# Optimization experiments

Hardware: AMD Instinct MI355X
Metric: run time of the kernel (lower is better)

Reference implementation:

```python
import jax, jax.numpy as jnp
import numpy as np

K = 512          # patch size
H = 16           # heads
C = 768          # dim
ROPE_BASE = 100.0
COUNTS = [8000, 8300, 7800, 8668]


def _build_pad_unpad(counts, k):
    # faithful numpy replica of EfficientAttentionV2.get_padding_and_inverse
    counts = np.asarray(counts, dtype=np.int64)
    cpad = np.where(counts > k, ((counts + k - 1) // k) * k, counts)
    off = np.concatenate([[0], np.cumsum(counts)])
    offp = np.concatenate([[0], np.cumsum(cpad)])
    pad = np.arange(offp[-1])
    unpad = np.arange(off[-1])
    for i in range(len(counts)):
        unpad[off[i]:off[i + 1]] += offp[i] - off[i]
        if counts[i] != cpad[i]:
            s = offp[i + 1] - k + counts[i] % k
            pad[s:offp[i + 1]] = pad[s - k:offp[i + 1] - k]
        pad[offp[i]:offp[i + 1]] -= offp[i] - off[i]
    return pad, unpad


def setup_inputs() -> dict:
    key = jax.random.key(0)
    ks = jax.random.split(key, 6)
    N = int(np.sum(COUNTS))
    pad, unpad = _build_pad_unpad(COUNTS, K)
    rng = np.random.default_rng(0)
    perm = rng.permutation(N)                 # serialized_order stand-in
    inv_perm = np.argsort(perm)               # serialized_inverse
    order = perm[pad].astype(np.int32)        # [N_pad]
    inverse = unpad[inv_perm].astype(np.int32)  # [N]
    grid = rng.integers(0, 1024, size=(N, 3))
    pos = grid[order].astype(np.int32)        # [N_pad, 3], gathered grid coords
    s = 0.02
    return {
        "x": jax.random.normal(ks[0], (N, C), jnp.float32),
        "w_qkv": jax.random.normal(ks[1], (C, 3 * C), jnp.float32) * s,
        "b_qkv": jnp.zeros((3 * C,), jnp.float32),
        "w_proj": jax.random.normal(ks[2], (C, C), jnp.float32) * s,
        "b_proj": jnp.zeros((C,), jnp.float32),
        "order": jnp.asarray(order),
        "inverse": jnp.asarray(inverse),
        "pos": jnp.asarray(pos),
    }


def _rope1d(tok, pos1d):
    # tok: [P, K, H, d], pos1d: [P, K]
    d = tok.shape[-1]
    inv_freq = 1.0 / (ROPE_BASE ** (jnp.arange(0, d, 2, dtype=jnp.float32) / d))
    fr = pos1d[..., None].astype(jnp.float32) * inv_freq      # [P, K, d/2]
    fr = jnp.concatenate([fr, fr], axis=-1)[:, :, None, :]    # [P, K, 1, d]
    x1, x2 = jnp.split(tok, 2, axis=-1)
    rot = jnp.concatenate([-x2, x1], axis=-1)
    return tok * jnp.cos(fr) + rot * jnp.sin(fr)


def _rope3d(tok, pos):
    # tok: [P, K, H, D]; pos: [P, K, 3]; split head dim into 3 axis chunks
    parts = jnp.split(tok, 3, axis=-1)
    return jnp.concatenate(
        [_rope1d(parts[i], pos[..., i]) for i in range(3)], axis=-1)


def reference(x, w_qkv, b_qkv, w_proj, b_proj, order, inverse, pos):
    D = C // H
    scale = D ** -0.5
    qkv = x @ w_qkv + b_qkv                     # [N, 3C]
    qkv = qkv[order]                            # [N_pad, 3C] patch gather
    qkv = qkv.reshape(-1, K, 3, H, D)           # [P, K, 3, H, D]
    q, k, v = qkv[:, :, 0], qkv[:, :, 1], qkv[:, :, 2]  # [P, K, H, D]
    ppos = pos.reshape(-1, K, 3)
    q = _rope3d(q, ppos)
    k = _rope3d(k, ppos)
    attn = jnp.einsum("pkhd,pmhd->phkm", q, k) * scale
    attn = jax.nn.softmax(attn, axis=-1)
    feat = jnp.einsum("phkm,pmhd->pkhd", attn, v).reshape(-1, C)  # [N_pad, C]
    feat = feat[inverse]                        # [N, C] scatter-back
    return feat @ w_proj + b_proj
```

## Files before the change

kernel.cpp:

```cpp
#include <hip/hip_runtime.h>
#include <stdint.h>

typedef short short8 __attribute__((ext_vector_type(8)));
typedef short short4v __attribute__((ext_vector_type(4)));
typedef float f32x4 __attribute__((ext_vector_type(4)));
typedef float f32x16 __attribute__((ext_vector_type(16)));

#define AS1C(p) ((const __attribute__((address_space(1))) unsigned int*)(p))
#define AS3(p)  ((__attribute__((address_space(3))) unsigned int*)(p))

__device__ __forceinline__ short f2bf(float f) {
  union { float f; unsigned u; } v; v.f = f;
  unsigned r = v.u + 0x7FFFu + ((v.u >> 16) & 1u);
  return (short)(r >> 16);
}

__global__ void k_cast_bf16(const float* __restrict__ src, short* __restrict__ dst, int n8) {
  const int i = blockIdx.x * 256 + threadIdx.x;
  if (i >= n8) return;
  const float4* s = (const float4*)src + (size_t)i * 2;
  const float4 a = s[0], b = s[1];
  short8 o;
  o[0] = f2bf(a.x); o[1] = f2bf(a.y); o[2] = f2bf(a.z); o[3] = f2bf(a.w);
  o[4] = f2bf(b.x); o[5] = f2bf(b.y); o[6] = f2bf(b.z); o[7] = f2bf(b.w);
  ((short8*)dst)[i] = o;
}

__global__ void k_transpose_cast(const float* __restrict__ src, short* __restrict__ dst,
                                 int R, int C) {
  __shared__ float t[32][33];
  const int tx = threadIdx.x & 31, ty = threadIdx.x >> 5;
  const int c0 = blockIdx.x * 32, r0 = blockIdx.y * 32;
#pragma unroll
  for (int j = 0; j < 4; ++j)
    t[ty + j * 8][tx] = src[(size_t)(r0 + ty + j * 8) * C + c0 + tx];
  __syncthreads();
#pragma unroll
  for (int j = 0; j < 4; ++j)
    dst[(size_t)(c0 + ty + j * 8) * R + r0 + tx] = f2bf(t[tx][ty + j * 8]);
}

__global__ __launch_bounds__(256, 2)
void k_gemm1(const short* __restrict__ x16, const short* __restrict__ wt,
             const float* __restrict__ bqkv, const int* __restrict__ order,
             const int* __restrict__ pos,
             short* __restrict__ Qp, short* __restrict__ Kp, short* __restrict__ VpT) {
  __shared__ short sA[128 * 64];
  __shared__ short sB[128 * 64];
  __shared__ int sOrd[128];

  const int tid = threadIdx.x;
  const int lane = tid & 63;
  const int wv = tid >> 6;
  const int wm = wv >> 1, wn = wv & 1;
  const int tm = blockIdx.x * 128;
  const int tn = blockIdx.y * 128;

  if (tid < 128) sOrd[tid] = order[tm + tid];
  __syncthreads();

  const char* srcA[4];
  const char* srcB[4];
  {
    const int rr = tid >> 3, ck = tid & 7;
    const int sc = (ck ^ (rr & 7)) * 16;
#pragma unroll
    for (int is = 0; is < 4; ++is) {
      srcA[is] = (const char*)(x16 + (size_t)sOrd[is * 32 + rr] * 768) + sc;
      srcB[is] = (const char*)(wt + (size_t)(tn + is * 32 + rr) * 768) + sc;
    }
  }

  f32x4 acc[4][4] = {};
  const int ldsw = wv << 10;

  for (int kk = 0; kk < 12; ++kk) {
    const int kb = kk << 7;
#pragma unroll
    for (int is = 0; is < 4; ++is)
      __builtin_amdgcn_global_load_lds(AS1C(srcA[is] + kb), AS3((char*)sA + is * 4096 + ldsw), 16, 0, 0);
#pragma unroll
    for (int is = 0; is < 4; ++is)
      __builtin_amdgcn_global_load_lds(AS1C(srcB[is] + kb), AS3((char*)sB + is * 4096 + ldsw), 16, 0, 0);
    __syncthreads();

#pragma unroll
    for (int kbl = 0; kbl < 2; ++kbl) {
      const int ko = kbl * 64 + ((lane >> 4) << 4);
      short8 af[4], bf[4];
#pragma unroll
      for (int mi = 0; mi < 4; ++mi) {
        int row = wm * 64 + mi * 16 + (lane & 15);
        af[mi] = *(const short8*)((const char*)sA + row * 128 + (ko ^ ((row & 7) << 4)));
      }
#pragma unroll
      for (int ni = 0; ni < 4; ++ni) {
        int row = wn * 64 + ni * 16 + (lane & 15);
        bf[ni] = *(const short8*)((const char*)sB + row * 128 + (ko ^ ((row & 7) << 4)));
      }
#pragma unroll
      for (int mi = 0; mi < 4; ++mi)
#pragma unroll
        for (int ni = 0; ni < 4; ++ni)
          acc[mi][ni] = __builtin_amdgcn_mfma_f32_16x16x32_bf16(af[mi], bf[ni], acc[mi][ni], 0, 0, 0);
    }
    __syncthreads();
  }

  const int which = tn / 768;
  if (which == 2) {
#pragma unroll
    for (int ni = 0; ni < 4; ++ni) {
      const int col = tn + wn * 64 + ni * 16 + (lane & 15);
      const int hcol = col - 1536;
      const int h = hcol / 48;
      const int dd = hcol % 48;
      const float bq = bqkv[col];
#pragma unroll
      for (int mi = 0; mi < 4; ++mi) {
        const int m0 = tm + wm * 64 + mi * 16 + ((lane >> 4) << 2);
        const int p = m0 >> 9, q0 = m0 & 511;
        short4v vv;
#pragma unroll
        for (int r = 0; r < 4; ++r) vv[r] = f2bf(acc[mi][ni][r] + bq);
        *(short4v*)(VpT + ((size_t)(p * 16 + h) * 48 + dd) * 512 + q0) = vv;
      }
    }
  } else {
    const float invf = exp2f(-(float)(lane & 7) * 0.830482023721840f);
#pragma unroll
    for (int ni = 0; ni < 4; ++ni) {
      const int col = tn + wn * 64 + ni * 16 + (lane & 15);
      const int hcol = col - which * 768;
      const int h = hcol / 48;
      const int dd = hcol % 48;
      const int part = dd >> 4;
      const float bq = bqkv[col];
#pragma unroll
      for (int mi = 0; mi < 4; ++mi) {
        const int m0 = tm + wm * 64 + mi * 16 + ((lane >> 4) << 2);
#pragma unroll
        for (int r = 0; r < 4; ++r) {
          const int m = m0 + r;
          float val = acc[mi][ni][r] + bq;
          const int pv = pos[m * 3 + part];
          float s, c;
          __sincosf((float)pv * invf, &s, &c);
          const float partner = __shfl_xor(val, 8);
          val = val * c + ((lane & 8) ? partner : -partner) * s;
          const int p = m >> 9, q = m & 511;
          const size_t ro = (size_t)(p * 16 + h) * 512 + q;
          if (which == 0) Qp[ro * 48 + dd] = f2bf(val);
          else            Kp[(ro << 6) + dd] = f2bf(val);
        }
      }
    }
  }
}

__global__ __launch_bounds__(512, 2)
void k_attn(const short* __restrict__ Qp, const short* __restrict__ Kp,
            const short* __restrict__ VpT, short* __restrict__ featp) {
  __shared__ short sK[2][64 * 64];
  __shared__ short sV[2][64 * 64];

  const int tid = threadIdx.x;
  const int lane = tid & 63;
  const int wv = tid >> 6;
  const int l31 = lane & 31;
  const int hi = lane >> 5;
  const int ph = blockIdx.x;
  const int p = ph >> 4, h = ph & 15;

  ((float*)((char*)sV[0] + 6144))[tid] = 0.0f;
  ((float*)((char*)sV[1] + 6144))[tid] = 0.0f;

  short8 qf[2][3];
  {
    const short* Qb = Qp + ((size_t)ph * 512 + wv * 64) * 48;
#pragma unroll
    for (int qt = 0; qt < 2; ++qt)
#pragma unroll
      for (int dk = 0; dk < 3; ++dk)
        qf[qt][dk] = *(const short8*)(Qb + (qt * 32 + l31) * 48 + dk * 16 + hi * 8);
  }

  const char* Kb = (const char*)Kp + (size_t)ph * 65536;
  const char* Vb = (const char*)VpT + (size_t)ph * 49152;
  const int ldsw = wv << 10;
  const int o = tid * 16;
  const int swK = o ^ ((o >> 3) & 0x70);
  const int dV = tid >> 3;
  const int inrowV = (o & 127) ^ ((o >> 3) & 0x70);

  auto stage = [&](int b, int ms) {
    __builtin_amdgcn_global_load_lds(AS1C(Kb + ms * 8192 + swK), AS3((char*)sK[b] + ldsw), 16, 0, 0);
    if (tid < 384)
      __builtin_amdgcn_global_load_lds(AS1C(Vb + (size_t)dV * 1024 + ms * 128 + inrowV),
                                       AS3((char*)sV[b] + ldsw), 16, 0, 0);
  };

  stage(0, 0);
  asm volatile("s_waitcnt vmcnt(0)" ::: "memory");
  __syncthreads();

  f32x16 O[2][2] = {};
  float lr[2] = {0.f, 0.f};
  const float K2 = 0.14433756729740644f * 1.4426950408889634f;
  const float MB = 8.0f * K2;

  for (int ms = 0; ms < 8; ++ms) {
    const int bb = ms & 1;
    if (ms < 7) stage(bb ^ 1, ms + 1);

    const char* kb = (const char*)sK[bb];
    const char* vb = (const char*)sV[bb];

    f32x16 st[2][2];
    {
      short8 kf[2][3];
#pragma unroll
      for (int mt = 0; mt < 2; ++mt) {
        const int row = mt * 32 + l31;
        const int swr = (row & 7) << 4;
#pragma unroll
        for (int dk = 0; dk < 3; ++dk) {
          const int ob = (dk * 16 + hi * 8) * 2;
          kf[mt][dk] = *(const short8*)(kb + row * 128 + (ob ^ swr));
        }
      }
      __builtin_amdgcn_s_setprio(1);
#pragma unroll
      for (int mt = 0; mt < 2; ++mt)
#pragma unroll
        for (int qt = 0; qt < 2; ++qt) {
          f32x16 a = {};
#pragma unroll
          for (int dk = 0; dk < 3; ++dk)
            a = __builtin_amdgcn_mfma_f32_32x32x16_bf16(kf[mt][dk], qf[qt][dk], a, 0, 0, 0);
          st[mt][qt] = a;
        }
      __builtin_amdgcn_s_setprio(0);
    }

    unsigned pk[2][2][8];
#pragma unroll
    for (int qt = 0; qt < 2; ++qt) {
      float ps = 0.f;
#pragma unroll
      for (int mt = 0; mt < 2; ++mt) {
#pragma unroll
        for (int pr = 0; pr < 8; ++pr) {
          float p0 = exp2f(st[mt][qt][pr * 2]     * K2 - MB);
          float p1 = exp2f(st[mt][qt][pr * 2 + 1] * K2 - MB);
          ps += p0 + p1;
          pk[mt][qt][pr] = (unsigned)(unsigned short)f2bf(p0) |
                           ((unsigned)(unsigned short)f2bf(p1) << 16);
        }
      }
      lr[qt] += ps;
    }

    short8 vf[2][4];
#pragma unroll
    for (int dt = 0; dt < 2; ++dt) {
      const int d = dt * 32 + l31;
      const int swr = (d & 7) << 4;
#pragma unroll
      for (int ks = 0; ks < 4; ++ks) {
        const int ob = (ks * 16 + hi * 8) * 2;
        vf[dt][ks] = *(const short8*)(vb + d * 128 + (ob ^ swr));
      }
    }
#pragma unroll
    for (int qt = 0; qt < 2; ++qt) {
#pragma unroll
      for (int ks = 0; ks < 4; ++ks) {
        const int mt = ks >> 1;
        const int b0 = (ks & 1) * 4;
        const unsigned X0 = pk[mt][qt][b0 + 0];
        const unsigned X1 = pk[mt][qt][b0 + 1];
        const unsigned Y0 = pk[mt][qt][b0 + 2];
        const unsigned Y1 = pk[mt][qt][b0 + 3];
        const unsigned tX0 = __shfl_xor(X0, 32);
        const unsigned tX1 = __shfl_xor(X1, 32);
        const unsigned tY0 = __shfl_xor(Y0, 32);
        const unsigned tY1 = __shfl_xor(Y1, 32);
        union { unsigned u[4]; short8 v; } aw;
        aw.u[0] = hi ? tY0 : X0;
        aw.u[1] = hi ? tY1 : X1;
        aw.u[2] = hi ? Y0 : tX0;
        aw.u[3] = hi ? Y1 : tX1;
        __builtin_amdgcn_s_setprio(1);
#pragma unroll
        for (int dt = 0; dt < 2; ++dt)
          O[qt][dt] = __builtin_amdgcn_mfma_f32_32x32x16_bf16(aw.v, vf[dt][ks], O[qt][dt], 0, 0, 0);
        __builtin_amdgcn_s_setprio(0);
      }
    }

    if (ms < 7) {
      asm volatile("s_waitcnt vmcnt(0)" ::: "memory");
      __syncthreads();
    }
  }

#pragma unroll
  for (int qt = 0; qt < 2; ++qt) {
    float l = lr[qt] + __shfl_xor(lr[qt], 32);
    const float il = 1.0f / l;
#pragma unroll
    for (int r = 0; r < 16; ++r) {
      const int crow = (r & 3) + ((r >> 2) << 3) + (hi << 2);
      const float ilr = __shfl(il, crow);
      const int qg = wv * 64 + qt * 32 + crow;
      const size_t base = ((size_t)(p * 512 + qg)) * 768 + h * 48;
      featp[base + l31] = f2bf(O[qt][0][r] * ilr);
      if (l31 < 16) featp[base + 32 + l31] = f2bf(O[qt][1][r] * ilr);
    }
  }
}

__global__ __launch_bounds__(256, 2)
void k_gemm2(const short* __restrict__ featp, const short* __restrict__ wt,
             const float* __restrict__ bproj, const int* __restrict__ inverse,
             float* __restrict__ out) {
  __shared__ short sA[128 * 64];
  __shared__ short sB[128 * 64];
  __shared__ int sInv[128];

  const int tid = threadIdx.x;
  const int lane = tid & 63;
  const int wv = tid >> 6;
  const int wm = wv >> 1, wn = wv & 1;
  const int tm = blockIdx.x * 128;
  const int tn = blockIdx.y * 128;

  if (tid < 128) sInv[tid] = inverse[tm + tid];
  __syncthreads();

  const char* srcA[4];
  const char* srcB[4];
  {
    const int rr = tid >> 3, ck = tid & 7;
    const int sc = (ck ^ (rr & 7)) * 16;
#pragma unroll
    for (int is = 0; is < 4; ++is) {
      srcA[is] = (const char*)(featp + (size_t)sInv[is * 32 + rr] * 768) + sc;
      srcB[is] = (const char*)(wt + (size_t)(tn + is * 32 + rr) * 768) + sc;
    }
  }

  f32x4 acc[4][4] = {};
  const int ldsw = wv << 10;

  for (int kk = 0; kk < 12; ++kk) {
    const int kb = kk << 7;
#pragma unroll
    for (int is = 0; is < 4; ++is)
      __builtin_amdgcn_global_load_lds(AS1C(srcA[is] + kb), AS3((char*)sA + is * 4096 + ldsw), 16, 0, 0);
#pragma unroll
    for (int is = 0; is < 4; ++is)
      __builtin_amdgcn_global_load_lds(AS1C(srcB[is] + kb), AS3((char*)sB + is * 4096 + ldsw), 16, 0, 0);
    __syncthreads();

#pragma unroll
    for (int kbl = 0; kbl < 2; ++kbl) {
      const int ko = kbl * 64 + ((lane >> 4) << 4);
      short8 af[4], bf[4];
#pragma unroll
      for (int mi = 0; mi < 4; ++mi) {
        int row = wm * 64 + mi * 16 + (lane & 15);
        af[mi] = *(const short8*)((const char*)sA + row * 128 + (ko ^ ((row & 7) << 4)));
      }
#pragma unroll
      for (int ni = 0; ni < 4; ++ni) {
        int row = wn * 64 + ni * 16 + (lane & 15);
        bf[ni] = *(const short8*)((const char*)sB + row * 128 + (ko ^ ((row & 7) << 4)));
      }
#pragma unroll
      for (int mi = 0; mi < 4; ++mi)
#pragma unroll
        for (int ni = 0; ni < 4; ++ni)
          acc[mi][ni] = __builtin_amdgcn_mfma_f32_16x16x32_bf16(af[mi], bf[ni], acc[mi][ni], 0, 0, 0);
    }
    __syncthreads();
  }

#pragma unroll
  for (int ni = 0; ni < 4; ++ni) {
    const int col = tn + wn * 64 + ni * 16 + (lane & 15);
    const float bq = bproj[col];
#pragma unroll
    for (int mi = 0; mi < 4; ++mi) {
      const int m0 = tm + wm * 64 + mi * 16 + ((lane >> 4) << 2);
#pragma unroll
      for (int r = 0; r < 4; ++r)
        out[(size_t)(m0 + r) * 768 + col] = acc[mi][ni][r] + bq;
    }
  }
}

extern "C" void kernel_launch(void* const* d_in, const int* in_sizes, int n_in,
                              void* d_out, int out_size, void* d_ws, size_t ws_size,
                              hipStream_t stream) {
  (void)n_in; (void)out_size; (void)ws_size;
  const float* x      = (const float*)d_in[0];
  const float* w_qkv  = (const float*)d_in[1];
  const float* b_qkv  = (const float*)d_in[2];
  const float* w_proj = (const float*)d_in[3];
  const float* b_proj = (const float*)d_in[4];
  const int* order    = (const int*)d_in[5];
  const int* inverse  = (const int*)d_in[6];
  const int* pos      = (const int*)d_in[7];
  float* out = (float*)d_out;

  const int N = in_sizes[6];
  const int Npad = in_sizes[5];

  char* ws = (char*)d_ws;
  const size_t szTok = (size_t)Npad * 768 * 2;
  short* x16   = (short*)ws;
  short* featp = (short*)ws;
  short* wt1 = (short*)(ws + szTok);
  short* wt2 = (short*)(ws + szTok + 3538944);
  short* Qp  = (short*)(ws + szTok + 3538944 + 1179648);
  short* Kp  = (short*)(ws + szTok * 2 + 3538944 + 1179648);
  short* VpT = (short*)(ws + szTok * 2 + 3538944 + 1179648 + (size_t)Npad * 2048);

  k_cast_bf16<<<dim3((N * 768 / 8 + 255) / 256), 256, 0, stream>>>(x, x16, N * 768 / 8);
  k_transpose_cast<<<dim3(2304 / 32, 768 / 32), 256, 0, stream>>>(w_qkv, wt1, 768, 2304);
  k_transpose_cast<<<dim3(768 / 32, 768 / 32), 256, 0, stream>>>(w_proj, wt2, 768, 768);
  k_gemm1<<<dim3(Npad / 128, 18), 256, 0, stream>>>(x16, wt1, b_qkv, order, pos, Qp, Kp, VpT);
  k_attn<<<dim3((Npad / 512) * 16), 512, 0, stream>>>(Qp, Kp, VpT, featp);
  k_gemm2<<<dim3(N / 128, 6), 256, 0, stream>>>(featp, wt2, b_proj, inverse, out);
}
```

Measured before the change: 444.2 us.

## Triple-buffer K/V staging in attention with one barrier per tile

Moves the attention kernel's K/V LDS staging from double to triple buffering, issuing loads two tiles ahead. It replaces the two full vmcnt(0)+syncthreads points per iteration with a partial vmcnt wait (depending on whether the wave issues V loads) and a single barrier. It also splits the softmax row-sum accumulator into two chains, switches the bf16 packing to the HIP bfloat162 conversion intrinsic, and fully unrolls the tile loop. This costs 16KB more LDS per block and relies on exact per-wave vmcnt bookkeeping, which could break if the compiler reorders loads.

```diff
diff --git a/kernel.cpp b/kernel.cpp
--- a/kernel.cpp
+++ b/kernel.cpp
@@ -1,4 +1,5 @@
 #include <hip/hip_runtime.h>
+#include <hip/hip_bf16.h>
 #include <stdint.h>
 
 typedef short short8 __attribute__((ext_vector_type(8)));
@@ -161,8 +162,8 @@
 __global__ __launch_bounds__(512, 2)
 void k_attn(const short* __restrict__ Qp, const short* __restrict__ Kp,
             const short* __restrict__ VpT, short* __restrict__ featp) {
-  __shared__ short sK[2][64 * 64];
-  __shared__ short sV[2][64 * 64];
+  __shared__ short sK[3][64 * 64];
+  __shared__ short sV[3][64 * 64];
 
   const int tid = threadIdx.x;
   const int lane = tid & 63;
@@ -172,8 +173,9 @@
   const int ph = blockIdx.x;
   const int p = ph >> 4, h = ph & 15;
 
-  ((float*)((char*)sV[0] + 6144))[tid] = 0.0f;
-  ((float*)((char*)sV[1] + 6144))[tid] = 0.0f;
+#pragma unroll
+  for (int b = 0; b < 3; ++b)
+    ((float*)((char*)sV[b] + 6144))[tid] = 0.0f;
 
   short8 qf[2][3];
   {
@@ -201,20 +203,28 @@
   };
 
   stage(0, 0);
-  asm volatile("s_waitcnt vmcnt(0)" ::: "memory");
-  __syncthreads();
+  stage(1, 1);
 
   f32x16 O[2][2] = {};
   float lr[2] = {0.f, 0.f};
   const float K2 = 0.14433756729740644f * 1.4426950408889634f;
   const float MB = 8.0f * K2;
 
+#pragma unroll
   for (int ms = 0; ms < 8; ++ms) {
-    const int bb = ms & 1;
-    if (ms < 7) stage(bb ^ 1, ms + 1);
-
-    const char* kb = (const char*)sK[bb];
-    const char* vb = (const char*)sV[bb];
+    if (wv < 6) {
+      if (ms < 7) asm volatile("s_waitcnt vmcnt(2)" ::: "memory");
+      else        asm volatile("s_waitcnt vmcnt(0)" ::: "memory");
+    } else {
+      if (ms < 7) asm volatile("s_waitcnt vmcnt(1)" ::: "memory");
+      else        asm volatile("s_waitcnt vmcnt(0)" ::: "memory");
+    }
+    if (ms == 0) asm volatile("s_waitcnt lgkmcnt(0)" ::: "memory");
+    __builtin_amdgcn_s_barrier();
+
+    if (ms < 6) stage((ms + 2) % 3, ms + 2);
+    const char* kb = (const char*)sK[ms % 3];
+    const char* vb = (const char*)sV[ms % 3];
 
     f32x16 st[2][2];
     {
@@ -246,19 +256,20 @@
     unsigned pk[2][2][8];
 #pragma unroll
     for (int qt = 0; qt < 2; ++qt) {
-      float ps = 0.f;
+      float ps0 = 0.f, ps1 = 0.f;
 #pragma unroll
       for (int mt = 0; mt < 2; ++mt) {
 #pragma unroll
         for (int pr = 0; pr < 8; ++pr) {
           float p0 = exp2f(st[mt][qt][pr * 2]     * K2 - MB);
           float p1 = exp2f(st[mt][qt][pr * 2 + 1] * K2 - MB);
-          ps += p0 + p1;
-          pk[mt][qt][pr] = (unsigned)(unsigned short)f2bf(p0) |
-                           ((unsigned)(unsigned short)f2bf(p1) << 16);
+          ps0 += p0; ps1 += p1;
+          __hip_bfloat162 bb = __float22bfloat162_rn(make_float2(p0, p1));
+          unsigned w; __builtin_memcpy(&w, &bb, 4);
+          pk[mt][qt][pr] = w;
         }
       }
-      lr[qt] += ps;
+      lr[qt] += ps0 + ps1;
     }
 
     short8 vf[2][4];
@@ -298,11 +309,6 @@
         __builtin_amdgcn_s_setprio(0);
       }
     }
-
-    if (ms < 7) {
-      asm volatile("s_waitcnt vmcnt(0)" ::: "memory");
-      __syncthreads();
-    }
   }
 
 #pragma unroll
```

New measurement: 1.065 ms. 2.4x slower.
